# Kernel optimization log

Measured on AMD Instinct MI355X. Metric: run time of the kernel, lower is better.

The kernel has to match this reference:

```python
import jax, jax.numpy as jnp
import numpy as np

DIM = 512
HEADS = 8
DIM_HEAD = 64
INNER = HEADS * DIM_HEAD  # 512
EPS_LN = 1e-5
EPS_Q = 1e-6


def ternary_quant(w):
    # BitNet-style ternary quantization: scale by mean |w|, round to {-1,0,1}
    s = jnp.mean(jnp.abs(w))
    return jnp.round(jnp.clip(w / (s + EPS_Q), -1.0, 1.0)) * s


def layernorm(x, g, b):
    mu = jnp.mean(x, axis=-1, keepdims=True)
    var = jnp.mean(jnp.square(x - mu), axis=-1, keepdims=True)
    return (x - mu) * jax.lax.rsqrt(var + EPS_LN) * g + b


def setup_inputs() -> dict:
    key = jax.random.key(0)
    ks = jax.random.split(key, 6)
    x = jax.random.normal(ks[0], (8, 1024, DIM), dtype=jnp.float32)
    W_qkv = jax.random.normal(ks[1], (3 * INNER, DIM), dtype=jnp.float32) * (DIM ** -0.5)
    W_out = jax.random.normal(ks[2], (DIM, INNER), dtype=jnp.float32) * (INNER ** -0.5)
    b_out = jnp.zeros((DIM,), dtype=jnp.float32)
    g1 = jnp.ones((DIM,), dtype=jnp.float32)
    b1 = jnp.zeros((DIM,), dtype=jnp.float32)
    g2 = jnp.ones((INNER,), dtype=jnp.float32)
    b2 = jnp.zeros((INNER,), dtype=jnp.float32)
    return {"x": x, "g1": g1, "b1": b1, "W_qkv": W_qkv, "g2": g2, "b2": b2, "W_out": W_out, "b_out": b_out}


def reference(x, g1, b1, W_qkv, g2, b2, W_out, b_out):
    b, n, _ = x.shape
    scale = DIM_HEAD ** -0.5
    x = layernorm(x, g1, b1)
    qkv = x @ ternary_quant(W_qkv).T  # [b, n, 3*inner]
    q, k, v = jnp.split(qkv, 3, axis=-1)
    # b n (h d) -> b h n d
    def split_heads(t):
        return t.reshape(b, n, HEADS, DIM_HEAD).transpose(0, 2, 1, 3)
    q, k, v = split_heads(q), split_heads(k), split_heads(v)
    attn_map = jnp.einsum('bhnd,bhmd->bhnm', q, k) * scale  # [b,h,n,n]
    attn = jax.nn.softmax(attn_map, axis=-1)
    out = jnp.einsum('bhnm,bhmd->bhnd', attn, v)
    out = out.transpose(0, 2, 1, 3).reshape(b, n, INNER)  # b n (h d)
    out = layernorm(out, g2, b2)
    out = out @ ternary_quant(W_out).T + b_out
    return out
```

## Files before the change

### kernel.cpp

```cpp
#include <hip/hip_runtime.h>
#include <hip/hip_bf16.h>

typedef __bf16 bf16x8 __attribute__((ext_vector_type(8)));
typedef float  f32x4  __attribute__((ext_vector_type(4)));

#define SEQ   1024
#define BATCH 8
#define DIMM  512
#define HEADS 8
#define DHEAD 64
#define TRIPLE 1536
#define MROWS (BATCH*SEQ)

#define GLOAD_LDS16(g, l) __builtin_amdgcn_global_load_lds( \
    (const __attribute__((address_space(1))) void*)(const void*)(g), \
    (__attribute__((address_space(3))) void*)(void*)(l), 16, 0, 0)

__global__ __launch_bounds__(256) void absum_all(const float* __restrict__ w1,
                                                 const float* __restrict__ w2,
                                                 float* __restrict__ part) {
    const int bid = blockIdx.x, tid = threadIdx.x;
    float s = 0.f;
    if (bid < 256) {
        const float4* p = (const float4*)w1;
        for (int i = bid * 256 + tid; i < 196608; i += 65536) {
            float4 v = p[i];
            s += fabsf(v.x) + fabsf(v.y) + fabsf(v.z) + fabsf(v.w);
        }
    } else {
        const float4* p = (const float4*)w2;
        for (int i = (bid - 256) * 256 + tid; i < 65536; i += 16384) {
            float4 v = p[i];
            s += fabsf(v.x) + fabsf(v.y) + fabsf(v.z) + fabsf(v.w);
        }
    }
    for (int o = 32; o; o >>= 1) s += __shfl_down(s, o);
    __shared__ float red[4];
    if (!(tid & 63)) red[tid >> 6] = s;
    __syncthreads();
    if (tid == 0) part[bid] = red[0] + red[1] + red[2] + red[3];
}

__global__ __launch_bounds__(256) void quant_all(const float* __restrict__ w1,
                                                 const float* __restrict__ w2,
                                                 const float* __restrict__ part,
                                                 __bf16* __restrict__ o1,
                                                 __bf16* __restrict__ o2) {
    const int bid = blockIdx.x, tid = threadIdx.x;
    float acc = 0.f;
    if (bid < 768) acc = part[tid];
    else if (tid < 64) acc = part[256 + tid];
    for (int o = 32; o; o >>= 1) acc += __shfl_down(acc, o);
    __shared__ float red[4];
    if (!(tid & 63)) red[tid >> 6] = acc;
    __syncthreads();
    const float tot = red[0] + red[1] + red[2] + red[3];
    const float s = (bid < 768) ? tot / 786432.0f : tot / 262144.0f;
    const float inv = 1.f / (s + 1e-6f);

    const float* w; __bf16* o; int idx;
    if (bid < 768) { w = w1; o = o1; idx = (bid * 256 + tid) * 4; }
    else           { w = w2; o = o2; idx = ((bid - 768) * 256 + tid) * 4; }
    float4 v = *reinterpret_cast<const float4*>(w + idx);
    o[idx + 0] = (__bf16)(rintf(fminf(1.f, fmaxf(-1.f, v.x * inv))) * s);
    o[idx + 1] = (__bf16)(rintf(fminf(1.f, fmaxf(-1.f, v.y * inv))) * s);
    o[idx + 2] = (__bf16)(rintf(fminf(1.f, fmaxf(-1.f, v.z * inv))) * s);
    o[idx + 3] = (__bf16)(rintf(fminf(1.f, fmaxf(-1.f, v.w * inv))) * s);
}

template<typename TIN>
__global__ __launch_bounds__(256) void ln_fast(const TIN* __restrict__ x,
                                               const float* __restrict__ g,
                                               const float* __restrict__ bta,
                                               __bf16* __restrict__ y) {
    const int row = blockIdx.x * 4 + (threadIdx.x >> 6);
    const int lane = threadIdx.x & 63;
    float v[8];
    if constexpr (sizeof(TIN) == 4) {
        const float4* xr = (const float4*)((const float*)x + (size_t)row * DIMM + lane * 8);
        float4 a = xr[0], bq = xr[1];
        v[0] = a.x; v[1] = a.y; v[2] = a.z; v[3] = a.w;
        v[4] = bq.x; v[5] = bq.y; v[6] = bq.z; v[7] = bq.w;
    } else {
        bf16x8 a = *reinterpret_cast<const bf16x8*>((const __bf16*)x + (size_t)row * DIMM + lane * 8);
#pragma unroll
        for (int e = 0; e < 8; ++e) v[e] = (float)a[e];
    }
    float s = 0.f, sq = 0.f;
#pragma unroll
    for (int e = 0; e < 8; ++e) { s += v[e]; sq += v[e] * v[e]; }
    for (int o = 32; o; o >>= 1) { s += __shfl_xor(s, o); sq += __shfl_xor(sq, o); }
    const float mu = s * (1.f / DIMM);
    const float invs = rsqrtf(sq * (1.f / DIMM) - mu * mu + 1e-5f);
    const float4* gp = (const float4*)(g + lane * 8);
    const float4* bp = (const float4*)(bta + lane * 8);
    float4 g0 = gp[0], g1 = gp[1], b0 = bp[0], b1 = bp[1];
    float o_[8] = {
        (v[0] - mu) * invs * g0.x + b0.x, (v[1] - mu) * invs * g0.y + b0.y,
        (v[2] - mu) * invs * g0.z + b0.z, (v[3] - mu) * invs * g0.w + b0.w,
        (v[4] - mu) * invs * g1.x + b1.x, (v[5] - mu) * invs * g1.y + b1.y,
        (v[6] - mu) * invs * g1.z + b1.z, (v[7] - mu) * invs * g1.w + b1.w };
    uint4 st;
    asm("v_cvt_pk_bf16_f32 %0, %1, %2" : "=v"(st.x) : "v"(o_[0]), "v"(o_[1]));
    asm("v_cvt_pk_bf16_f32 %0, %1, %2" : "=v"(st.y) : "v"(o_[2]), "v"(o_[3]));
    asm("v_cvt_pk_bf16_f32 %0, %1, %2" : "=v"(st.z) : "v"(o_[4]), "v"(o_[5]));
    asm("v_cvt_pk_bf16_f32 %0, %1, %2" : "=v"(st.w) : "v"(o_[6]), "v"(o_[7]));
    *reinterpret_cast<uint4*>(y + (size_t)row * DIMM + lane * 8) = st;
}

template<int NCOLS, bool BIAS, bool OUT_F32>
__global__ __launch_bounds__(256) void gemm_lds(const __bf16* __restrict__ A,
                                                const __bf16* __restrict__ Wt,
                                                const float* __restrict__ bias,
                                                __bf16* __restrict__ outb,
                                                float* __restrict__ outf) {
    const int K = DIMM;
    __shared__ __align__(16) __bf16 As[2][4096];
    __shared__ __align__(16) __bf16 Bs[2][4096];

    const int tid = threadIdx.x;
    const int w = tid >> 6, lane = tid & 63;
    const int m = lane & 15, g = lane >> 4;
    const int mi = w >> 1, ni = w & 1;

    const int trow = tid >> 2;
    const int tc = tid & 3;
    const int sc = (tc ^ ((trow >> 1) & 3)) * 8;
    const __bf16* a0 = A  + (size_t)(blockIdx.x * 128 + trow) * K + sc;
    const __bf16* a1 = a0 + (size_t)64 * K;
    const __bf16* b0 = Wt + (size_t)(blockIdx.y * 128 + trow) * K + sc;
    const __bf16* b1 = b0 + (size_t)64 * K;

    f32x4 acc[4][4] = {};

    GLOAD_LDS16(a0, (char*)As[0] + tid * 16);
    GLOAD_LDS16(a1, (char*)As[0] + 4096 + tid * 16);
    GLOAD_LDS16(b0, (char*)Bs[0] + tid * 16);
    GLOAD_LDS16(b1, (char*)Bs[0] + 4096 + tid * 16);

    int cur = 0;
    for (int k0 = 0; k0 < K; k0 += 32) {
        __syncthreads();
        if (k0 + 32 < K) {
            GLOAD_LDS16(a0 + k0 + 32, (char*)As[cur ^ 1] + tid * 16);
            GLOAD_LDS16(a1 + k0 + 32, (char*)As[cur ^ 1] + 4096 + tid * 16);
            GLOAD_LDS16(b0 + k0 + 32, (char*)Bs[cur ^ 1] + tid * 16);
            GLOAD_LDS16(b1 + k0 + 32, (char*)Bs[cur ^ 1] + 4096 + tid * 16);
        }

        const char* Ab = (const char*)As[cur];
        const char* Bb = (const char*)Bs[cur];
        bf16x8 af[4], bfr[4];
#pragma unroll
        for (int i = 0; i < 4; ++i) {
            const int ra = mi * 64 + i * 16 + m;
            af[i] = *reinterpret_cast<const bf16x8*>(Ab + ra * 64 + ((g ^ ((ra >> 1) & 3)) << 4));
        }
#pragma unroll
        for (int j = 0; j < 4; ++j) {
            const int rb = ni * 64 + j * 16 + m;
            bfr[j] = *reinterpret_cast<const bf16x8*>(Bb + rb * 64 + ((g ^ ((rb >> 1) & 3)) << 4));
        }
#pragma unroll
        for (int i = 0; i < 4; ++i)
#pragma unroll
            for (int j = 0; j < 4; ++j)
                acc[i][j] = __builtin_amdgcn_mfma_f32_16x16x32_bf16(af[i], bfr[j], acc[i][j], 0, 0, 0);
        cur ^= 1;
    }

    const int orow0 = blockIdx.x * 128 + mi * 64 + g * 4;
    const int ocol0 = blockIdx.y * 128 + ni * 64;
#pragma unroll
    for (int i = 0; i < 4; ++i)
#pragma unroll
        for (int j = 0; j < 4; ++j)
#pragma unroll
            for (int r = 0; r < 4; ++r) {
                int row = orow0 + i * 16 + r;
                int col = ocol0 + j * 16 + m;
                float v = acc[i][j][r];
                if (BIAS) v += bias[col];
                if (OUT_F32) outf[(size_t)row * NCOLS + col] = v;
                else         outb[(size_t)row * NCOLS + col] = (__bf16)v;
            }
}

__global__ __launch_bounds__(256, 4) void attn_mfma(const __bf16* __restrict__ qkv,
                                                    __bf16* __restrict__ out) {
    const int qt = blockIdx.y, bh = blockIdx.x;
    const int b = bh >> 3, h = bh & 7;
    const int tid = threadIdx.x;
    const int w = tid >> 6, lane = tid & 63;
    const int g = lane >> 4, m = lane & 15;

    __shared__ __align__(16) __bf16 Kb[4096];
    __shared__ __align__(16) __bf16 Vt[4096];
    __shared__ __align__(16) __bf16 Pl[4][1024];

    bf16x8 qf[2];
    {
        const __bf16* qp = qkv + (size_t)(b * SEQ + qt * 64 + w * 16 + m) * TRIPLE + h * 64 + g * 8;
        qf[0] = *reinterpret_cast<const bf16x8*>(qp);
        qf[1] = *reinterpret_cast<const bf16x8*>(qp + 32);
#pragma unroll
        for (int e = 0; e < 8; ++e) {
            qf[0][e] = (__bf16)((float)qf[0][e] * 0.125f);
            qf[1][e] = (__bf16)((float)qf[1][e] * 0.125f);
        }
    }

    const int srow = tid >> 3;
    const int sc   = tid & 7;
    const size_t rbase = (size_t)(b * SEQ + srow) * TRIPLE + h * 64 + sc * 8;
    const __bf16* k0s = qkv + rbase + DIMM;
    const __bf16* v0s = qkv + rbase + 2 * DIMM;
    const __bf16* k1s = k0s + (size_t)32 * TRIPLE;
    const __bf16* v1s = v0s + (size_t)32 * TRIPLE;
    const int kstep = 64 * TRIPLE;

    char* kw0 = (char*)Kb + srow * 128 + ((sc ^ (srow & 7)) << 4);
    char* kw1 = kw0 + 32 * 128;
    char* vbp = (char*)Vt;

    f32x4 oa[4] = {};
    float mrun = -1e30f, lrun = 0.f;

    uint4 k0c = *reinterpret_cast<const uint4*>(k0s);
    uint4 k1c = *reinterpret_cast<const uint4*>(k1s);
    uint4 v0c = *reinterpret_cast<const uint4*>(v0s);
    uint4 v1c = *reinterpret_cast<const uint4*>(v1s);
    uint4 k0n = {}, k1n = {}, v0n = {}, v1n = {};

    for (int t = 0; t < 16; ++t) {
        __syncthreads();

        *reinterpret_cast<bf16x8*>(kw0) = *reinterpret_cast<bf16x8*>(&k0c);
        *reinterpret_cast<bf16x8*>(kw1) = *reinterpret_cast<bf16x8*>(&k1c);
        {
            bf16x8 va = *reinterpret_cast<bf16x8*>(&v0c);
            bf16x8 vb = *reinterpret_cast<bf16x8*>(&v1c);
#pragma unroll
            for (int e = 0; e < 8; ++e) {
                const int dro = (sc * 8 + e) * 128;
                const int sw = ((sc ^ e) & 7) << 4;
                *(__bf16*)(vbp + dro + ((srow * 2) ^ sw))        = va[e];
                *(__bf16*)(vbp + dro + (((srow + 32) * 2) ^ sw)) = vb[e];
            }
        }
        __syncthreads();

        if (t < 15) {
            k0n = *reinterpret_cast<const uint4*>(k0s + (size_t)(t + 1) * kstep);
            k1n = *reinterpret_cast<const uint4*>(k1s + (size_t)(t + 1) * kstep);
            v0n = *reinterpret_cast<const uint4*>(v0s + (size_t)(t + 1) * kstep);
            v1n = *reinterpret_cast<const uint4*>(v1s + (size_t)(t + 1) * kstep);
        }

        const char* kb = (const char*)Kb;
        f32x4 sa[4];
#pragma unroll
        for (int i = 0; i < 4; ++i) sa[i] = (f32x4){0.f, 0.f, 0.f, 0.f};
#pragma unroll
        for (int kc = 0; kc < 2; ++kc) {
            const int cp = ((kc * 4 + g) ^ (m & 7)) << 4;
#pragma unroll
            for (int i = 0; i < 4; ++i) {
                bf16x8 kf = *reinterpret_cast<const bf16x8*>(kb + (i * 16 + m) * 128 + cp);
                sa[i] = __builtin_amdgcn_mfma_f32_16x16x32_bf16(kf, qf[kc], sa[i], 0, 0, 0);
            }
        }

        char* pw = (char*)Pl[w] + m * 128;
        const int psw = (m & 7) << 4;
        {
            float mx = -1e30f;
#pragma unroll
            for (int i = 0; i < 4; ++i)
#pragma unroll
                for (int r = 0; r < 4; ++r) mx = fmaxf(mx, sa[i][r]);
            mx = fmaxf(mx, __shfl_xor(mx, 16));
            mx = fmaxf(mx, __shfl_xor(mx, 32));
            const float mnew = fmaxf(mrun, mx);
            float p[4][4];
            float ps = 0.f;
#pragma unroll
            for (int i = 0; i < 4; ++i)
#pragma unroll
                for (int r = 0; r < 4; ++r) { p[i][r] = __expf(sa[i][r] - mnew); ps += p[i][r]; }
            ps += __shfl_xor(ps, 16);
            ps += __shfl_xor(ps, 32);
            const float al = __expf(mrun - mnew);
            mrun = mnew;
            lrun = lrun * al + ps;
#pragma unroll
            for (int i = 0; i < 4; ++i)
#pragma unroll
                for (int r = 0; r < 4; ++r) oa[i][r] *= al;
#pragma unroll
            for (int i = 0; i < 4; ++i) {
                uint2 pk;
                asm("v_cvt_pk_bf16_f32 %0, %1, %2" : "=v"(pk.x) : "v"(p[i][0]), "v"(p[i][1]));
                asm("v_cvt_pk_bf16_f32 %0, %1, %2" : "=v"(pk.y) : "v"(p[i][2]), "v"(p[i][3]));
                *reinterpret_cast<uint2*>(pw + ((i * 32 + g * 8) ^ psw)) = pk;
            }
        }

        bf16x8 pf[2];
#pragma unroll
        for (int kc = 0; kc < 2; ++kc)
            pf[kc] = *reinterpret_cast<const bf16x8*>(pw + ((kc * 64 + g * 16) ^ psw));

#pragma unroll
        for (int kc = 0; kc < 2; ++kc)
#pragma unroll
            for (int i = 0; i < 4; ++i) {
                const int sv = ((i * 2 + (m >> 3)) ^ (m & 7)) & 7;
                bf16x8 vf = *reinterpret_cast<const bf16x8*>(
                    vbp + (i * 16 + m) * 128 + (((kc * 4 + g) ^ sv) << 4));
                oa[i] = __builtin_amdgcn_mfma_f32_16x16x32_bf16(vf, pf[kc], oa[i], 0, 0, 0);
            }

        k0c = k0n; k1c = k1n; v0c = v0n; v1c = v1n;
    }

    const float inv = 1.0f / lrun;
    unsigned int* orow = (unsigned int*)(out +
        (size_t)(b * SEQ + qt * 64 + w * 16 + m) * DIMM + h * 64);
#pragma unroll
    for (int i = 0; i < 4; ++i)
#pragma unroll
        for (int rp = 0; rp < 2; ++rp) {
            float o0 = oa[i][2 * rp] * inv, o1 = oa[i][2 * rp + 1] * inv;
            unsigned int pk;
            asm("v_cvt_pk_bf16_f32 %0, %1, %2" : "=v"(pk) : "v"(o0), "v"(o1));
            orow[i * 8 + g * 2 + rp] = pk;
        }
}

extern "C" void kernel_launch(void* const* d_in, const int* in_sizes, int n_in,
                              void* d_out, int out_size, void* d_ws, size_t ws_size,
                              hipStream_t stream) {
    const float* x     = (const float*)d_in[0];
    const float* g1    = (const float*)d_in[1];
    const float* b1    = (const float*)d_in[2];
    const float* W_qkv = (const float*)d_in[3];
    const float* g2    = (const float*)d_in[4];
    const float* b2    = (const float*)d_in[5];
    const float* W_out = (const float*)d_in[6];
    const float* b_out = (const float*)d_in[7];
    float* out = (float*)d_out;

    char* ws = (char*)d_ws;
    float* part   = (float*)(ws);
    __bf16* Wq1 = (__bf16*)(ws + 4096);
    __bf16* Wq2 = (__bf16*)(ws + 4096 + 1572864);
    __bf16* Xln = (__bf16*)(ws + 4096 + 1572864 + 524288);
    __bf16* QKV = (__bf16*)(ws + 4096 + 1572864 + 524288 + 8388608);
    __bf16* AO  = (__bf16*)(ws + 4096 + 1572864 + 524288 + 8388608 + 25165824);

    absum_all<<<320, 256, 0, stream>>>(W_qkv, W_out, part);
    quant_all<<<1024, 256, 0, stream>>>(W_qkv, W_out, part, Wq1, Wq2);
    ln_fast<float><<<MROWS / 4, 256, 0, stream>>>(x, g1, b1, Xln);
    gemm_lds<TRIPLE, false, false><<<dim3(64, 12), 256, 0, stream>>>(Xln, Wq1, nullptr, QKV, nullptr);
    attn_mfma<<<dim3(64, 16), 256, 0, stream>>>(QKV, AO);
    ln_fast<__bf16><<<MROWS / 4, 256, 0, stream>>>(AO, g2, b2, Xln);
    gemm_lds<DIMM, true, true><<<dim3(64, 4), 256, 0, stream>>>(Xln, Wq2, b_out, nullptr, out);
}
```

Baseline: 89.82 us.

## Pre-transpose V globally and load K/V fragments directly from global memory in attention

Adds a separate kernel that transposes V per head into a head-major [d, seq] buffer, reusing the Xln workspace. The attention kernel then drops K/V LDS staging and both block barriers per tile, and each wave reads its K and V MFMA fragments straight from global memory (L2/cache). This removes LDS write traffic, the scalar V scatter and synchronisation, but each of the four waves now fetches the full K/V tiles redundantly from global memory, without software prefetch, and adds an extra kernel launch plus a V round trip.

```diff
diff --git a/kernel.cpp b/kernel.cpp
--- a/kernel.cpp
+++ b/kernel.cpp
@@ -186,16 +186,44 @@
             }
 }
 
-__global__ __launch_bounds__(256, 4) void attn_mfma(const __bf16* __restrict__ qkv,
-                                                    __bf16* __restrict__ out) {
-    const int qt = blockIdx.y, bh = blockIdx.x;
+__global__ __launch_bounds__(256) void transpose_v(const __bf16* __restrict__ qkv,
+                                                   __bf16* __restrict__ vtg) {
+    __shared__ __align__(16) __bf16 Vl[4096];
+    const int bh = blockIdx.x, nt = blockIdx.y;
+    const int b = bh >> 3, h = bh & 7;
+    const int tid = threadIdx.x;
+    const int r = tid >> 3, c = tid & 7;
+    const __bf16* src = qkv + (size_t)(b * SEQ + nt * 64 + r) * TRIPLE + 2 * DIMM + h * 64 + c * 8;
+    uint4 v0 = *reinterpret_cast<const uint4*>(src);
+    uint4 v1 = *reinterpret_cast<const uint4*>(src + (size_t)32 * TRIPLE);
+    char* lp = (char*)Vl;
+    *reinterpret_cast<uint4*>(lp + r * 128 + ((c ^ (r & 7)) << 4)) = v0;
+    *reinterpret_cast<uint4*>(lp + (r + 32) * 128 + ((c ^ (r & 7)) << 4)) = v1;
+    __syncthreads();
+    const int d = tid >> 2, qtr = tid & 3;
+    const int cd = d >> 3, dby = (d & 7) * 2;
+    unsigned un[8];
+#pragma unroll
+    for (int s2 = 0; s2 < 8; ++s2) {
+        const int tok0 = qtr * 16 + s2 * 2, tok1 = tok0 + 1;
+        unsigned lo = *reinterpret_cast<const unsigned short*>(lp + tok0 * 128 + ((cd ^ (tok0 & 7)) << 4) + dby);
+        unsigned hi = *reinterpret_cast<const unsigned short*>(lp + tok1 * 128 + ((cd ^ (tok1 & 7)) << 4) + dby);
+        un[s2] = lo | (hi << 16);
+    }
+    __bf16* dst = vtg + (size_t)(bh * 64 + d) * SEQ + nt * 64 + qtr * 16;
+    *reinterpret_cast<uint4*>(dst)     = make_uint4(un[0], un[1], un[2], un[3]);
+    *reinterpret_cast<uint4*>(dst + 8) = make_uint4(un[4], un[5], un[6], un[7]);
+}
+
+__global__ __launch_bounds__(256) void attn_g(const __bf16* __restrict__ qkv,
+                                              const __bf16* __restrict__ vtg,
+                                              __bf16* __restrict__ out) {
+    const int bh = blockIdx.x, qt = blockIdx.y;
     const int b = bh >> 3, h = bh & 7;
     const int tid = threadIdx.x;
     const int w = tid >> 6, lane = tid & 63;
     const int g = lane >> 4, m = lane & 15;
 
-    __shared__ __align__(16) __bf16 Kb[4096];
-    __shared__ __align__(16) __bf16 Vt[4096];
     __shared__ __align__(16) __bf16 Pl[4][1024];
 
     bf16x8 qf[2];
@@ -210,69 +238,33 @@
         }
     }
 
-    const int srow = tid >> 3;
-    const int sc   = tid & 7;
-    const size_t rbase = (size_t)(b * SEQ + srow) * TRIPLE + h * 64 + sc * 8;
-    const __bf16* k0s = qkv + rbase + DIMM;
-    const __bf16* v0s = qkv + rbase + 2 * DIMM;
-    const __bf16* k1s = k0s + (size_t)32 * TRIPLE;
-    const __bf16* v1s = v0s + (size_t)32 * TRIPLE;
-    const int kstep = 64 * TRIPLE;
-
-    char* kw0 = (char*)Kb + srow * 128 + ((sc ^ (srow & 7)) << 4);
-    char* kw1 = kw0 + 32 * 128;
-    char* vbp = (char*)Vt;
+    const __bf16* kb = qkv + (size_t)(b * SEQ + m) * TRIPLE + DIMM + h * 64 + g * 8;
+    const __bf16* vb = vtg + (size_t)(bh * 64 + m) * SEQ + g * 8;
 
     f32x4 oa[4] = {};
     float mrun = -1e30f, lrun = 0.f;
 
-    uint4 k0c = *reinterpret_cast<const uint4*>(k0s);
-    uint4 k1c = *reinterpret_cast<const uint4*>(k1s);
-    uint4 v0c = *reinterpret_cast<const uint4*>(v0s);
-    uint4 v1c = *reinterpret_cast<const uint4*>(v1s);
-    uint4 k0n = {}, k1n = {}, v0n = {}, v1n = {};
+    char* pw = (char*)Pl[w] + m * 128;
+    const int psw = (m & 7) << 4;
 
     for (int t = 0; t < 16; ++t) {
-        __syncthreads();
-
-        *reinterpret_cast<bf16x8*>(kw0) = *reinterpret_cast<bf16x8*>(&k0c);
-        *reinterpret_cast<bf16x8*>(kw1) = *reinterpret_cast<bf16x8*>(&k1c);
-        {
-            bf16x8 va = *reinterpret_cast<bf16x8*>(&v0c);
-            bf16x8 vb = *reinterpret_cast<bf16x8*>(&v1c);
-#pragma unroll
-            for (int e = 0; e < 8; ++e) {
-                const int dro = (sc * 8 + e) * 128;
-                const int sw = ((sc ^ e) & 7) << 4;
-                *(__bf16*)(vbp + dro + ((srow * 2) ^ sw))        = va[e];
-                *(__bf16*)(vbp + dro + (((srow + 32) * 2) ^ sw)) = vb[e];
-            }
-        }
-        __syncthreads();
-
-        if (t < 15) {
-            k0n = *reinterpret_cast<const uint4*>(k0s + (size_t)(t + 1) * kstep);
-            k1n = *reinterpret_cast<const uint4*>(k1s + (size_t)(t + 1) * kstep);
-            v0n = *reinterpret_cast<const uint4*>(v0s + (size_t)(t + 1) * kstep);
-            v1n = *reinterpret_cast<const uint4*>(v1s + (size_t)(t + 1) * kstep);
-        }
-
-        const char* kb = (const char*)Kb;
+        bf16x8 kf[2][4];
+#pragma unroll
+        for (int kc = 0; kc < 2; ++kc)
+#pragma unroll
+            for (int i = 0; i < 4; ++i)
+                kf[kc][i] = *reinterpret_cast<const bf16x8*>(
+                    kb + (size_t)(t * 64 + i * 16) * TRIPLE + kc * 32);
+
         f32x4 sa[4];
 #pragma unroll
         for (int i = 0; i < 4; ++i) sa[i] = (f32x4){0.f, 0.f, 0.f, 0.f};
 #pragma unroll
-        for (int kc = 0; kc < 2; ++kc) {
-            const int cp = ((kc * 4 + g) ^ (m & 7)) << 4;
-#pragma unroll
-            for (int i = 0; i < 4; ++i) {
-                bf16x8 kf = *reinterpret_cast<const bf16x8*>(kb + (i * 16 + m) * 128 + cp);
-                sa[i] = __builtin_amdgcn_mfma_f32_16x16x32_bf16(kf, qf[kc], sa[i], 0, 0, 0);
-            }
-        }
-
-        char* pw = (char*)Pl[w] + m * 128;
-        const int psw = (m & 7) << 4;
+        for (int kc = 0; kc < 2; ++kc)
+#pragma unroll
+            for (int i = 0; i < 4; ++i)
+                sa[i] = __builtin_amdgcn_mfma_f32_16x16x32_bf16(kf[kc][i], qf[kc], sa[i], 0, 0, 0);
+
         {
             float mx = -1e30f;
 #pragma unroll
@@ -311,17 +303,19 @@
         for (int kc = 0; kc < 2; ++kc)
             pf[kc] = *reinterpret_cast<const bf16x8*>(pw + ((kc * 64 + g * 16) ^ psw));
 
-#pragma unroll
-        for (int kc = 0; kc < 2; ++kc)
-#pragma unroll
-            for (int i = 0; i < 4; ++i) {
-                const int sv = ((i * 2 + (m >> 3)) ^ (m & 7)) & 7;
-                bf16x8 vf = *reinterpret_cast<const bf16x8*>(
-                    vbp + (i * 16 + m) * 128 + (((kc * 4 + g) ^ sv) << 4));
-                oa[i] = __builtin_amdgcn_mfma_f32_16x16x32_bf16(vf, pf[kc], oa[i], 0, 0, 0);
-            }
-
-        k0c = k0n; k1c = k1n; v0c = v0n; v1c = v1n;
+        bf16x8 vf[2][4];
+#pragma unroll
+        for (int kc = 0; kc < 2; ++kc)
+#pragma unroll
+            for (int i = 0; i < 4; ++i)
+                vf[kc][i] = *reinterpret_cast<const bf16x8*>(
+                    vb + (size_t)(i * 16) * SEQ + t * 64 + kc * 32);
+
+#pragma unroll
+        for (int kc = 0; kc < 2; ++kc)
+#pragma unroll
+            for (int i = 0; i < 4; ++i)
+                oa[i] = __builtin_amdgcn_mfma_f32_16x16x32_bf16(vf[kc][i], pf[kc], oa[i], 0, 0, 0);
     }
 
     const float inv = 1.0f / lrun;
@@ -358,12 +352,14 @@
     __bf16* Xln = (__bf16*)(ws + 4096 + 1572864 + 524288);
     __bf16* QKV = (__bf16*)(ws + 4096 + 1572864 + 524288 + 8388608);
     __bf16* AO  = (__bf16*)(ws + 4096 + 1572864 + 524288 + 8388608 + 25165824);
+    __bf16* VT  = Xln;
 
     absum_all<<<320, 256, 0, stream>>>(W_qkv, W_out, part);
     quant_all<<<1024, 256, 0, stream>>>(W_qkv, W_out, part, Wq1, Wq2);
     ln_fast<float><<<MROWS / 4, 256, 0, stream>>>(x, g1, b1, Xln);
     gemm_lds<TRIPLE, false, false><<<dim3(64, 12), 256, 0, stream>>>(Xln, Wq1, nullptr, QKV, nullptr);
-    attn_mfma<<<dim3(64, 16), 256, 0, stream>>>(QKV, AO);
+    transpose_v<<<dim3(64, 16), 256, 0, stream>>>(QKV, VT);
+    attn_g<<<dim3(64, 16), 256, 0, stream>>>(QKV, VT, AO);
     ln_fast<__bf16><<<MROWS / 4, 256, 0, stream>>>(AO, g2, b2, Xln);
     gemm_lds<DIMM, true, true><<<dim3(64, 4), 256, 0, stream>>>(Xln, Wq2, b_out, nullptr, out);
 }
```

New measurement: 201.3 us. 124% more time.
